# Kernel tuning notes

Hardware: AMD Instinct MI355X
Metric: run time of the kernel (lower is better)

Reference implementation:

```python
import jax, jax.numpy as jnp
import numpy as np

IN_F = 4096
OUT_F = 11008
GROUPSIZE = 128
N_GROUPS = IN_F // GROUPSIZE  # 32


def setup_inputs() -> dict:
    key = jax.random.key(0)
    k1, k2, k3, k4 = jax.random.split(key, 4)
    x = jax.random.normal(k1, (4, 2048, IN_F), dtype=jnp.float32)
    # packed 4-bit weights: 8 nibbles per int32 along the input dim
    qweight = jax.random.randint(k2, (IN_F // 8, OUT_F), 0, 2**31 - 1, dtype=jnp.int32)
    # packed 4-bit zero points: 8 nibbles per int32 along the output dim
    qzeros = jax.random.randint(k3, (N_GROUPS, OUT_F // 8), 0, 2**31 - 1, dtype=jnp.int32)
    scales = jax.random.uniform(k4, (N_GROUPS, OUT_F), dtype=jnp.float32,
                                minval=0.001, maxval=0.01)
    g_idx = (jnp.arange(IN_F, dtype=jnp.int32) // GROUPSIZE).astype(jnp.int32)
    return {"x": x, "qweight": qweight, "scales": scales,
            "qzeros": qzeros, "g_idx": g_idx}


def _dequantize(qweight, scales, qzeros, g_idx):
    """GPTQ v2 dequant: W[i, j] = scales[g_idx[i], j] * (q[i, j] - (z[g_idx[i], j] + 1))."""
    shifts = jnp.arange(8, dtype=jnp.int32) * 4  # nibble shift amounts
    # unpack weights along input dim: [in/8, 8, out] -> [in, out]
    q = (qweight[:, None, :] >> shifts[None, :, None]) & 0xF
    q = q.reshape(-1, qweight.shape[1]).astype(scales.dtype)
    # unpack zeros along output dim: [g, out/8, 8] -> [g, out]; +1 per GPTQ v2
    z = ((qzeros[:, :, None] >> shifts[None, None, :]) & 0xF) + 1
    z = z.reshape(qzeros.shape[0], -1).astype(scales.dtype)
    return scales[g_idx] * (q - z[g_idx])  # [in, out]


def reference(x, qweight, scales, qzeros, g_idx):
    W = _dequantize(qweight, scales, qzeros, g_idx)  # [IN_F, OUT_F]
    return jnp.einsum('bsi,io->bso', x, W)
```

## Files before the change

kernel.cpp:

```cpp
#include <hip/hip_runtime.h>
#include <hip/hip_bf16.h>

#define IN_F 4096
#define OUT_F 11008

typedef __bf16 bf16_t;
typedef bf16_t bf16x8 __attribute__((ext_vector_type(8)));
typedef float f32x4 __attribute__((ext_vector_type(4)));

#define BM 128
#define BN 128
#define BK 32
#define LDP 48

__global__ __launch_bounds__(256, 2) void gptq_gemm_kernel(
    const float* __restrict__ x,
    const int*   __restrict__ qweight,
    const float* __restrict__ scales,
    const int*   __restrict__ qzeros,
    float* __restrict__ out)
{
    __shared__ bf16_t As[BM * LDP];
    __shared__ bf16_t Bs[BN * LDP];

    const int tid  = threadIdx.x;
    const int lane = tid & 63;
    const int wid  = tid >> 6;
    const int wr   = wid >> 1;
    const int wc   = wid & 1;

    const int m0 = blockIdx.y * BM;
    const int n0 = blockIdx.x * BN;

    const int a_row  = tid >> 2;
    const int a_slot = tid & 3;
    const int b_k8l = tid >> 7;
    const int b_n   = tid & 127;

    f32x4 acc[4][4];
    #pragma unroll
    for (int i = 0; i < 4; ++i)
        #pragma unroll
        for (int j = 0; j < 4; ++j)
            acc[i][j] = (f32x4)0.0f;

    for (int kt = 0; kt < IN_F / BK; ++kt) {
        const int k0 = kt * BK;
        const int g  = k0 >> 7;

        __syncthreads();

        #pragma unroll
        for (int p = 0; p < 2; ++p) {
            const int row = a_row + p * 64;
            const float* src = x + (size_t)(m0 + row) * IN_F + k0 + a_slot * 8;
            f32x4 v0 = *(const f32x4*)src;
            f32x4 v1 = *(const f32x4*)(src + 4);
            bf16x8 h;
            h[0] = (bf16_t)v0[0]; h[1] = (bf16_t)v0[1];
            h[2] = (bf16_t)v0[2]; h[3] = (bf16_t)v0[3];
            h[4] = (bf16_t)v1[0]; h[5] = (bf16_t)v1[1];
            h[6] = (bf16_t)v1[2]; h[7] = (bf16_t)v1[3];
            *(bf16x8*)(&As[row * LDP + a_slot * 8]) = h;
        }

        {
            const int n  = b_n;
            const int gn = n0 + n;
            const float s  = scales[(size_t)g * OUT_F + gn];
            const int   zw = qzeros[(size_t)g * (OUT_F / 8) + (gn >> 3)];
            const float z1 = (float)(((zw >> ((gn & 7) * 4)) & 0xF) + 1);
            const float sz = s * z1;
            #pragma unroll
            for (int p = 0; p < 2; ++p) {
                const int k8l = b_k8l + p * 2;
                const int w = qweight[(size_t)(k0 / 8 + k8l) * OUT_F + gn];
                bf16x8 h;
                #pragma unroll
                for (int j = 0; j < 8; ++j) {
                    const int q = (w >> (4 * j)) & 0xF;
                    h[j] = (bf16_t)fmaf((float)q, s, -sz);
                }
                *(bf16x8*)(&Bs[n * LDP + k8l * 8]) = h;
            }
        }

        __syncthreads();

        bf16x8 af[4], bfr[4];
        #pragma unroll
        for (int m = 0; m < 4; ++m) {
            const int row = wr * 64 + m * 16 + (lane & 15);
            af[m] = *(const bf16x8*)(&As[row * LDP + (lane >> 4) * 8]);
        }
        #pragma unroll
        for (int n = 0; n < 4; ++n) {
            const int col = wc * 64 + n * 16 + (lane & 15);
            bfr[n] = *(const bf16x8*)(&Bs[col * LDP + (lane >> 4) * 8]);
        }
        #pragma unroll
        for (int m = 0; m < 4; ++m)
            #pragma unroll
            for (int n = 0; n < 4; ++n)
                acc[m][n] = __builtin_amdgcn_mfma_f32_16x16x32_bf16(
                    af[m], bfr[n], acc[m][n], 0, 0, 0);
    }

    const int cn  = lane & 15;
    const int cr4 = (lane >> 4) * 4;
    #pragma unroll
    for (int m = 0; m < 4; ++m) {
        #pragma unroll
        for (int r = 0; r < 4; ++r) {
            const int grow = m0 + wr * 64 + m * 16 + cr4 + r;
            float* orow = out + (size_t)grow * OUT_F + n0 + wc * 64 + cn;
            #pragma unroll
            for (int n = 0; n < 4; ++n)
                orow[n * 16] = acc[m][n][r];
        }
    }
}

extern "C" void kernel_launch(void* const* d_in, const int* in_sizes, int n_in,
                              void* d_out, int out_size, void* d_ws, size_t ws_size,
                              hipStream_t stream) {
    const float* x       = (const float*)d_in[0];
    const int*   qweight = (const int*)d_in[1];
    const float* scales  = (const float*)d_in[2];
    const int*   qzeros  = (const int*)d_in[3];
    float* out = (float*)d_out;

    const int M = in_sizes[0] / IN_F;
    dim3 grid(OUT_F / BN, M / BM);
    dim3 block(256);
    gptq_gemm_kernel<<<grid, block, 0, stream>>>(x, qweight, scales, qzeros, out);
}
```

Before: 1.001 ms.

## Split into x conversion, one-shot weight dequant, and bf16 GEMM via LDS loads

Adds a pre-pass that converts x to bf16 and one that dequantizes the packed 4-bit weights into a transposed bf16 matrix in workspace. A separate GEMM then loads tiles directly into LDS with global_load_lds. This removes the redundant per-tile dequantization repeated by every M block, in exchange for extra global memory traffic and launches. It falls back to the fused kernel when workspace is too small.

New measurement: 1.293 ms. 1.29x slower.

```diff
diff --git a/kernel.cpp b/kernel.cpp
--- a/kernel.cpp
+++ b/kernel.cpp
@@ -7,35 +7,61 @@
 typedef __bf16 bf16_t;
 typedef bf16_t bf16x8 __attribute__((ext_vector_type(8)));
 typedef float f32x4 __attribute__((ext_vector_type(4)));
+typedef unsigned int u32;
+
+__global__ __launch_bounds__(256) void cvt_x_kernel(const float* __restrict__ x,
+                                                    bf16_t* __restrict__ xb) {
+    size_t i = ((size_t)blockIdx.x * 256 + threadIdx.x) * 8;
+    f32x4 v0 = *(const f32x4*)(x + i);
+    f32x4 v1 = *(const f32x4*)(x + i + 4);
+    bf16x8 h;
+    h[0]=(bf16_t)v0[0]; h[1]=(bf16_t)v0[1]; h[2]=(bf16_t)v0[2]; h[3]=(bf16_t)v0[3];
+    h[4]=(bf16_t)v1[0]; h[5]=(bf16_t)v1[1]; h[6]=(bf16_t)v1[2]; h[7]=(bf16_t)v1[3];
+    *(bf16x8*)(xb + i) = h;
+}
+
+__global__ __launch_bounds__(256) void dequant_kernel(const int* __restrict__ qweight,
+                                                      const float* __restrict__ scales,
+                                                      const int* __restrict__ qzeros,
+                                                      bf16_t* __restrict__ wt) {
+    const int n   = blockIdx.x * 256 + threadIdx.x;
+    const int kw0 = blockIdx.y * 4;
+    const int g   = kw0 >> 4;
+    const float s  = scales[(size_t)g * OUT_F + n];
+    const int   zw = qzeros[(size_t)g * (OUT_F / 8) + (n >> 3)];
+    const float nsz = -s * (float)(((zw >> ((n & 7) * 4)) & 0xF) + 1);
+    bf16_t* dst = wt + (size_t)n * IN_F + kw0 * 8;
+    #pragma unroll
+    for (int j = 0; j < 4; ++j) {
+        const int w = qweight[(size_t)(kw0 + j) * OUT_F + n];
+        bf16x8 h;
+        #pragma unroll
+        for (int b = 0; b < 8; ++b)
+            h[b] = (bf16_t)fmaf((float)((w >> (4 * b)) & 0xF), s, nsz);
+        *(bf16x8*)(dst + j * 8) = h;
+    }
+}
 
 #define BM 128
 #define BN 128
 #define BK 32
-#define LDP 48
-
-__global__ __launch_bounds__(256, 2) void gptq_gemm_kernel(
-    const float* __restrict__ x,
-    const int*   __restrict__ qweight,
-    const float* __restrict__ scales,
-    const int*   __restrict__ qzeros,
-    float* __restrict__ out)
-{
-    __shared__ bf16_t As[BM * LDP];
-    __shared__ bf16_t Bs[BN * LDP];
+
+__global__ __launch_bounds__(256) void gemm_bt_kernel(const bf16_t* __restrict__ A,
+                                                      const bf16_t* __restrict__ B,
+                                                      float* __restrict__ C) {
+    __shared__ bf16_t As[BM * BK];
+    __shared__ bf16_t Bs[BN * BK];
 
     const int tid  = threadIdx.x;
     const int lane = tid & 63;
     const int wid  = tid >> 6;
     const int wr   = wid >> 1;
     const int wc   = wid & 1;
-
-    const int m0 = blockIdx.y * BM;
-    const int n0 = blockIdx.x * BN;
-
-    const int a_row  = tid >> 2;
-    const int a_slot = tid & 3;
-    const int b_k8l = tid >> 7;
-    const int b_n   = tid & 127;
+    const int m0   = blockIdx.y * BM;
+    const int n0   = blockIdx.x * BN;
+
+    const int s_row = tid >> 2;
+    const int s_k8  = tid & 3;
 
     f32x4 acc[4][4];
     #pragma unroll
@@ -43,13 +69,83 @@
         #pragma unroll
         for (int j = 0; j < 4; ++j)
             acc[i][j] = (f32x4)0.0f;
+
+    for (int kt = 0; kt < IN_F / BK; ++kt) {
+        const int k0 = kt * BK;
+        __syncthreads();
+
+        #pragma unroll
+        for (int p = 0; p < 2; ++p) {
+            const bf16_t* ga = A + (size_t)(m0 + s_row + p * 64) * IN_F + k0 + s_k8 * 8;
+            __builtin_amdgcn_global_load_lds(
+                (const __attribute__((address_space(1))) u32*)ga,
+                (__attribute__((address_space(3))) u32*)(As + ((p * 256 + wid * 64) * 8)),
+                16, 0, 0);
+            const bf16_t* gb = B + (size_t)(n0 + s_row + p * 64) * IN_F + k0 + s_k8 * 8;
+            __builtin_amdgcn_global_load_lds(
+                (const __attribute__((address_space(1))) u32*)gb,
+                (__attribute__((address_space(3))) u32*)(Bs + ((p * 256 + wid * 64) * 8)),
+                16, 0, 0);
+        }
+
+        __syncthreads();
+
+        bf16x8 af[4], bfr[4];
+        const int kslot = (lane >> 4) * 8;
+        #pragma unroll
+        for (int m = 0; m < 4; ++m)
+            af[m] = *(const bf16x8*)(As + (wr * 64 + m * 16 + (lane & 15)) * BK + kslot);
+        #pragma unroll
+        for (int n = 0; n < 4; ++n)
+            bfr[n] = *(const bf16x8*)(Bs + (wc * 64 + n * 16 + (lane & 15)) * BK + kslot);
+        #pragma unroll
+        for (int m = 0; m < 4; ++m)
+            #pragma unroll
+            for (int n = 0; n < 4; ++n)
+                acc[m][n] = __builtin_amdgcn_mfma_f32_16x16x32_bf16(
+                    af[m], bfr[n], acc[m][n], 0, 0, 0);
+    }
+
+    const int cn  = lane & 15;
+    const int cr4 = (lane >> 4) * 4;
+    #pragma unroll
+    for (int m = 0; m < 4; ++m) {
+        #pragma unroll
+        for (int r = 0; r < 4; ++r) {
+            const int grow = m0 + wr * 64 + m * 16 + cr4 + r;
+            float* orow = C + (size_t)grow * OUT_F + n0 + wc * 64 + cn;
+            #pragma unroll
+            for (int n = 0; n < 4; ++n)
+                orow[n * 16] = acc[m][n][r];
+        }
+    }
+}
+
+#define LDPF 40
+
+__global__ __launch_bounds__(256, 2) void gptq_gemm_fused(
+    const float* __restrict__ x, const int* __restrict__ qweight,
+    const float* __restrict__ scales, const int* __restrict__ qzeros,
+    float* __restrict__ out)
+{
+    __shared__ bf16_t As[BM * LDPF];
+    __shared__ bf16_t Bs[BN * LDPF];
+    const int tid = threadIdx.x, lane = tid & 63, wid = tid >> 6;
+    const int wr = wid >> 1, wc = wid & 1;
+    const int m0 = blockIdx.y * BM, n0 = blockIdx.x * BN;
+    const int a_row = tid >> 2, a_slot = tid & 3;
+    const int b_k8l = tid >> 7, b_n = tid & 127;
+
+    f32x4 acc[4][4];
+    #pragma unroll
+    for (int i = 0; i < 4; ++i)
+        #pragma unroll
+        for (int j = 0; j < 4; ++j) acc[i][j] = (f32x4)0.0f;
 
     for (int kt = 0; kt < IN_F / BK; ++kt) {
         const int k0 = kt * BK;
         const int g  = k0 >> 7;
-
-        __syncthreads();
-
+        __syncthreads();
         #pragma unroll
         for (int p = 0; p < 2; ++p) {
             const int row = a_row + p * 64;
@@ -57,68 +153,50 @@
             f32x4 v0 = *(const f32x4*)src;
             f32x4 v1 = *(const f32x4*)(src + 4);
             bf16x8 h;
-            h[0] = (bf16_t)v0[0]; h[1] = (bf16_t)v0[1];
-            h[2] = (bf16_t)v0[2]; h[3] = (bf16_t)v0[3];
-            h[4] = (bf16_t)v1[0]; h[5] = (bf16_t)v1[1];
-            h[6] = (bf16_t)v1[2]; h[7] = (bf16_t)v1[3];
-            *(bf16x8*)(&As[row * LDP + a_slot * 8]) = h;
-        }
-
+            h[0]=(bf16_t)v0[0]; h[1]=(bf16_t)v0[1]; h[2]=(bf16_t)v0[2]; h[3]=(bf16_t)v0[3];
+            h[4]=(bf16_t)v1[0]; h[5]=(bf16_t)v1[1]; h[6]=(bf16_t)v1[2]; h[7]=(bf16_t)v1[3];
+            *(bf16x8*)(&As[row * LDPF + a_slot * 8]) = h;
+        }
         {
-            const int n  = b_n;
-            const int gn = n0 + n;
+            const int gn = n0 + b_n;
             const float s  = scales[(size_t)g * OUT_F + gn];
             const int   zw = qzeros[(size_t)g * (OUT_F / 8) + (gn >> 3)];
-            const float z1 = (float)(((zw >> ((gn & 7) * 4)) & 0xF) + 1);
-            const float sz = s * z1;
+            const float sz = s * (float)(((zw >> ((gn & 7) * 4)) & 0xF) + 1);
             #pragma unroll
             for (int p = 0; p < 2; ++p) {
                 const int k8l = b_k8l + p * 2;
                 const int w = qweight[(size_t)(k0 / 8 + k8l) * OUT_F + gn];
                 bf16x8 h;
                 #pragma unroll
-                for (int j = 0; j < 8; ++j) {
-                    const int q = (w >> (4 * j)) & 0xF;
-                    h[j] = (bf16_t)fmaf((float)q, s, -sz);
-                }
-                *(bf16x8*)(&Bs[n * LDP + k8l * 8]) = h;
+                for (int j = 0; j < 8; ++j)
+                    h[j] = (bf16_t)fmaf((float)((w >> (4 * j)) & 0xF), s, -sz);
+                *(bf16x8*)(&Bs[b_n * LDPF + k8l * 8]) = h;
             }
         }
-
-        __syncthreads();
-
+        __syncthreads();
         bf16x8 af[4], bfr[4];
         #pragma unroll
-        for (int m = 0; m < 4; ++m) {
-            const int row = wr * 64 + m * 16 + (lane & 15);
-            af[m] = *(const bf16x8*)(&As[row * LDP + (lane >> 4) * 8]);
-        }
-        #pragma unroll
-        for (int n = 0; n < 4; ++n) {
-            const int col = wc * 64 + n * 16 + (lane & 15);
-            bfr[n] = *(const bf16x8*)(&Bs[col * LDP + (lane >> 4) * 8]);
-        }
+        for (int m = 0; m < 4; ++m)
+            af[m] = *(const bf16x8*)(&As[(wr * 64 + m * 16 + (lane & 15)) * LDPF + (lane >> 4) * 8]);
+        #pragma unroll
+        for (int n = 0; n < 4; ++n)
+            bfr[n] = *(const bf16x8*)(&Bs[(wc * 64 + n * 16 + (lane & 15)) * LDPF + (lane >> 4) * 8]);
         #pragma unroll
         for (int m = 0; m < 4; ++m)
             #pragma unroll
             for (int n = 0; n < 4; ++n)
-                acc[m][n] = __builtin_amdgcn_mfma_f32_16x16x32_bf16(
-                    af[m], bfr[n], acc[m][n], 0, 0, 0);
-    }
-
-    const int cn  = lane & 15;
-    const int cr4 = (lane >> 4) * 4;
-    #pragma unroll
-    for (int m = 0; m < 4; ++m) {
+                acc[m][n] = __builtin_amdgcn_mfma_f32_16x16x32_bf16(af[m], bfr[n], acc[m][n], 0, 0, 0);
+    }
+    const int cn = lane & 15, cr4 = (lane >> 4) * 4;
+    #pragma unroll
+    for (int m = 0; m < 4; ++m)
         #pragma unroll
         for (int r = 0; r < 4; ++r) {
             const int grow = m0 + wr * 64 + m * 16 + cr4 + r;
             float* orow = out + (size_t)grow * OUT_F + n0 + wc * 64 + cn;
             #pragma unroll
-            for (int n = 0; n < 4; ++n)
-                orow[n * 16] = acc[m][n][r];
-        }
-    }
+            for (int n = 0; n < 4; ++n) orow[n * 16] = acc[m][n][r];
+        }
 }
 
 extern "C" void kernel_launch(void* const* d_in, const int* in_sizes, int n_in,
@@ -131,7 +209,18 @@
     float* out = (float*)d_out;
 
     const int M = in_sizes[0] / IN_F;
-    dim3 grid(OUT_F / BN, M / BM);
-    dim3 block(256);
-    gptq_gemm_kernel<<<grid, block, 0, stream>>>(x, qweight, scales, qzeros, out);
-}
+    const size_t xb_bytes = (size_t)M * IN_F * 2;
+    const size_t wt_bytes = (size_t)IN_F * OUT_F * 2;
+
+    if (ws_size >= xb_bytes + wt_bytes) {
+        bf16_t* xb = (bf16_t*)d_ws;
+        bf16_t* wt = (bf16_t*)((char*)d_ws + xb_bytes);
+        cvt_x_kernel<<<dim3((M * IN_F) / (256 * 8)), dim3(256), 0, stream>>>(x, xb);
+        dequant_kernel<<<dim3(OUT_F / 256, IN_F / 32), dim3(256), 0, stream>>>(
+            qweight, scales, qzeros, wt);
+        gemm_bt_kernel<<<dim3(OUT_F / BN, M / BM), dim3(256), 0, stream>>>(xb, wt, out);
+    } else {
+        gptq_gemm_fused<<<dim3(OUT_F / BN, M / BM), dim3(256), 0, stream>>>(
+            x, qweight, scales, qzeros, out);
+    }
+}
```
